# Kernel tuning notes

Hardware: AMD Instinct MI355X
Metric: run time of the kernel (lower is better)

## Reference

```python
import jax, jax.numpy as jnp
import numpy as np

S, R, CM, CZ, H = 128, 256, 256, 128, 8
HD = CM // H
INF = 1e9
EPS = 1e-5


def _ln(x, g, b):
    mu = jnp.mean(x, axis=-1, keepdims=True)
    var = jnp.var(x, axis=-1, keepdims=True)
    return (x - mu) * jax.lax.rsqrt(var + EPS) * g + b


def setup_inputs() -> dict:
    key = jax.random.key(0)
    ks = jax.random.split(key, 12)
    d = {
        'm': jax.random.normal(ks[0], (S, R, CM), jnp.float32),
        'z': jax.random.normal(ks[1], (R, R, CZ), jnp.float32),
        'mask': jnp.ones((S, R), jnp.float32),
        'ln_m_g': jnp.ones((CM,), jnp.float32),
        'ln_m_b': jnp.zeros((CM,), jnp.float32),
        'ln_z_g': jnp.ones((CZ,), jnp.float32),
        'ln_z_b': jnp.zeros((CZ,), jnp.float32),
        'w_z': jax.random.normal(ks[2], (CZ, H), jnp.float32) * 0.02,
        'wq': jax.random.normal(ks[3], (CM, CM), jnp.float32) * (1.0 / np.sqrt(CM)),
        'wk': jax.random.normal(ks[4], (CM, CM), jnp.float32) * (1.0 / np.sqrt(CM)),
        'wv': jax.random.normal(ks[5], (CM, CM), jnp.float32) * (1.0 / np.sqrt(CM)),
        'wg': jnp.zeros((CM, CM), jnp.float32),
        'bg': jnp.ones((CM,), jnp.float32),
        'wo': jax.random.normal(ks[6], (CM, CM), jnp.float32) * (1.0 / np.sqrt(CM)),
        'bo': jnp.zeros((CM,), jnp.float32),
    }
    return d


def reference(m, z, mask, ln_m_g, ln_m_b, ln_z_g, ln_z_b, w_z, wq, wk, wv, wg, bg, wo, bo):
    # pair bias: LN(z) -> per-head bias [H, R, R], broadcast over seq rows
    z_ln = _ln(z, ln_z_g, ln_z_b)
    pair_bias = jnp.einsum('ijc,ch->hij', z_ln, w_z)          # [H, R, R]
    mask_bias = (INF * (mask - 1.0))[:, None, None, :]        # [S, 1, 1, R]

    m_ln = _ln(m, ln_m_g, ln_m_b)                             # [S, R, CM]
    q = (m_ln @ wq).reshape(S, R, H, HD)
    k = (m_ln @ wk).reshape(S, R, H, HD)
    v = (m_ln @ wv).reshape(S, R, H, HD)

    scale = 1.0 / np.sqrt(HD).astype(np.float32)
    logits = jnp.einsum('sihd,sjhd->shij', q * scale, k)       # [S, H, R, R]
    logits = logits + pair_bias[None] + mask_bias
    attn = jax.nn.softmax(logits, axis=-1)

    o = jnp.einsum('shij,sjhd->sihd', attn, v).reshape(S, R, CM)
    g = jax.nn.sigmoid(m_ln @ wg + bg)
    return (g * o) @ wo + bo
```

## Files before the change

kernel.cpp:

```cpp
#include <hip/hip_runtime.h>
#include <hip/hip_bf16.h>

typedef unsigned short u16;
typedef __bf16 bf16x8 __attribute__((ext_vector_type(8)));
typedef float f32x4 __attribute__((ext_vector_type(4)));
typedef float f32x16 __attribute__((ext_vector_type(16)));
typedef unsigned short u16x8 __attribute__((ext_vector_type(8)));
typedef unsigned short u16x4 __attribute__((ext_vector_type(4)));

#define LOG2E 1.4426950408889634f

__device__ __forceinline__ u16 f2b(float f) {
  union { __bf16 b; u16 u; } v; v.b = (__bf16)f; return v.u;
}
__device__ __forceinline__ float bf2f(u16 u) {
  union { unsigned u; float f; } v; v.u = ((unsigned)u) << 16;
  return v.f;
}

__global__ __launch_bounds__(256) void k_pre(
    const float* __restrict__ wq, const float* __restrict__ wk,
    const float* __restrict__ wv, const float* __restrict__ wg,
    const float* __restrict__ wo, u16* __restrict__ wtp,
    const float* __restrict__ z, const float* __restrict__ zg,
    const float* __restrict__ zb, const float* __restrict__ wz,
    float* __restrict__ pbp,
    const float* __restrict__ m, const float* __restrict__ gam,
    const float* __restrict__ bet, u16* __restrict__ mln) {
  __shared__ float lt[64][68];
  const int b = blockIdx.x;
  const int t = threadIdx.x;
  if (b < 80) {
    const int widx = b >> 4;
    const int tid = b & 15;
    const int ri = (tid >> 2) * 64, ci = (tid & 3) * 64;
    const float* src = (widx == 0) ? wq : (widx == 1) ? wk : (widx == 2) ? wv
                      : (widx == 3) ? wg : wo;
    {
      const int r = t >> 2;
      #pragma unroll
      for (int i = 0; i < 4; ++i) {
        const int c = (t & 3) * 16 + i * 4;
        *(float4*)&lt[r][c] = *(const float4*)&src[(ri + r) * 256 + ci + c];
      }
    }
    __syncthreads();
    #pragma unroll
    for (int cc = 0; cc < 2; ++cc) {
      const int c = t + cc * 256;
      const int kb = c >> 8, cb = (c >> 6) & 3, lg = (c >> 4) & 3, lr = c & 15;
      u16x8 o;
      #pragma unroll
      for (int j = 0; j < 8; ++j) o[j] = f2b(lt[kb * 32 + lg * 8 + j][cb * 16 + lr]);
      const size_t idx = (size_t)widx * 65536 + (size_t)((ci >> 4) + cb) * 4096
                       + (size_t)((ri >> 5) + kb) * 512 + (size_t)(lg * 16 + lr) * 8;
      *(u16x8*)&wtp[idx] = o;
    }
  } else if (b < 4176) {
    const int lane = t & 63, wave = t >> 6;
    const int ql = lane & 15;
    const int p = (b - 80) * 16 + wave * 4 + (lane >> 4);
    const float4 zv0 = *(const float4*)(z + (size_t)p * 128 + ql * 8);
    const float4 zv1 = *(const float4*)(z + (size_t)p * 128 + ql * 8 + 4);
    float s = zv0.x + zv0.y + zv0.z + zv0.w + zv1.x + zv1.y + zv1.z + zv1.w;
    float sq = zv0.x * zv0.x + zv0.y * zv0.y + zv0.z * zv0.z + zv0.w * zv0.w
             + zv1.x * zv1.x + zv1.y * zv1.y + zv1.z * zv1.z + zv1.w * zv1.w;
    #pragma unroll
    for (int o = 8; o > 0; o >>= 1) { s += __shfl_xor(s, o); sq += __shfl_xor(sq, o); }
    const float mu = s * 0.0078125f;
    const float var = sq * 0.0078125f - mu * mu;
    const float rs = rsqrtf(var + 1e-5f);
    const int c0 = ql * 8;
    float zn[8];
    zn[0] = (zv0.x - mu) * rs * zg[c0 + 0] + zb[c0 + 0];
    zn[1] = (zv0.y - mu) * rs * zg[c0 + 1] + zb[c0 + 1];
    zn[2] = (zv0.z - mu) * rs * zg[c0 + 2] + zb[c0 + 2];
    zn[3] = (zv0.w - mu) * rs * zg[c0 + 3] + zb[c0 + 3];
    zn[4] = (zv1.x - mu) * rs * zg[c0 + 4] + zb[c0 + 4];
    zn[5] = (zv1.y - mu) * rs * zg[c0 + 5] + zb[c0 + 5];
    zn[6] = (zv1.z - mu) * rs * zg[c0 + 6] + zb[c0 + 6];
    zn[7] = (zv1.w - mu) * rs * zg[c0 + 7] + zb[c0 + 7];
    float a[8] = {};
    #pragma unroll
    for (int i = 0; i < 8; ++i) {
      #pragma unroll
      for (int hh = 0; hh < 8; ++hh) a[hh] += zn[i] * wz[(c0 + i) * 8 + hh];
    }
    #pragma unroll
    for (int hh = 0; hh < 8; ++hh) {
      #pragma unroll
      for (int o = 8; o > 0; o >>= 1) a[hh] += __shfl_xor(a[hh], o);
    }
    if (ql == 0) {
      const int i = p >> 8, j = p & 255;
      const int strip = i >> 5, il = i & 31, jt = j >> 5, r = j & 31;
      const int gh = (r >> 2) & 1, qd = r >> 3, c4 = r & 3;
      const int off = (strip * 8 + jt) * 1024 + (gh * 32 + il) * 16 + qd * 4 + c4;
      #pragma unroll
      for (int hh = 0; hh < 8; ++hh)
        pbp[(size_t)hh * 65536 + off] = a[hh] * LOG2E;
    }
  } else {
    const int lane = t & 63;
    const size_t row = (size_t)(b - 4176) * 4 + (t >> 6);
    const float4 xv = *(const float4*)(m + row * 256 + lane * 4);
    float s = xv.x + xv.y + xv.z + xv.w;
    float sq = xv.x * xv.x + xv.y * xv.y + xv.z * xv.z + xv.w * xv.w;
    #pragma unroll
    for (int o = 32; o > 0; o >>= 1) { s += __shfl_xor(s, o); sq += __shfl_xor(sq, o); }
    const float mu = s * 0.00390625f;
    const float var = sq * 0.00390625f - mu * mu;
    const float rs = rsqrtf(var + 1e-5f);
    const int c = lane * 4;
    u16x4 o4;
    o4.x = f2b((xv.x - mu) * rs * gam[c] + bet[c]);
    o4.y = f2b((xv.y - mu) * rs * gam[c + 1] + bet[c + 1]);
    o4.z = f2b((xv.z - mu) * rs * gam[c + 2] + bet[c + 2]);
    o4.w = f2b((xv.w - mu) * rs * gam[c + 3] + bet[c + 3]);
    *(u16x4*)(mln + row * 256 + c) = o4;
  }
}

__global__ __launch_bounds__(256, 2) void k_fused(
    const u16* __restrict__ mln, const u16* __restrict__ wtp,
    const float* __restrict__ bg, const float* __restrict__ pbp,
    const float* __restrict__ mask, u16* __restrict__ go) {
  __shared__ u16 lA[32 * 256];
  __shared__ u16 lQ[256 * 32];
  __shared__ u16 lK[256 * 32];
  __shared__ u16 lVt[32][276];
  __shared__ float lMb[256];
  __shared__ float lL[4][32];
  const int bid = blockIdx.x;
  const int s = bid & 127, h = bid >> 7;
  const int t = threadIdx.x;
  const int lane = t & 63, wave = t >> 6;
  const int il = lane & 31, gh = lane >> 5;

  const u16* Wb = wtp + (size_t)wave * 65536 + (size_t)(2 * h + (il >> 4)) * 4096
                + gh * 128 + (il & 15) * 8;
  bf16x8 B[16];
  #pragma unroll
  for (int kc = 0; kc < 16; ++kc) B[kc] = *(const bf16x8*)&Wb[kc * 256];
  __builtin_amdgcn_sched_barrier(0);

  lMb[t] = (LOG2E * 1e9f) * (mask[s * 256 + t] - 1.0f) - 24.0f;
  const float bgv = bg[h * 32 + il];
  const size_t mbase = (size_t)s * 65536;

  u16x8 areg[4];
  #pragma unroll
  for (int i = 0; i < 4; ++i)
    areg[i] = *(const u16x8*)&mln[mbase + (size_t)(i * 8 + (t >> 5)) * 256 + (t & 31) * 8];
  unsigned gpk[64];

  #pragma unroll
  for (int c = 0; c < 8; ++c) {
    #pragma unroll
    for (int i = 0; i < 4; ++i) {
      const int r = i * 8 + (t >> 5);
      *(u16x8*)((char*)lA + ((r * 512 + (t & 31) * 16) ^ ((r & 7) << 4))) = areg[i];
    }
    __syncthreads();
    if (c < 7) {
      #pragma unroll
      for (int i = 0; i < 4; ++i)
        areg[i] = *(const u16x8*)&mln[mbase +
            (size_t)((c + 1) * 32 + i * 8 + (t >> 5)) * 256 + (t & 31) * 8];
      __builtin_amdgcn_sched_barrier(0);
    }
    f32x16 a0 = {}, a1 = {};
    #pragma unroll
    for (int kc = 0; kc < 16; kc += 2) {
      const bf16x8 af0 = *(const bf16x8*)((const char*)lA +
          ((il * 512 + (kc * 16 + gh * 8) * 2) ^ ((il & 7) << 4)));
      const bf16x8 af1 = *(const bf16x8*)((const char*)lA +
          ((il * 512 + ((kc + 1) * 16 + gh * 8) * 2) ^ ((il & 7) << 4)));
      a0 = __builtin_amdgcn_mfma_f32_32x32x16_bf16(af0, B[kc], a0, 0, 0, 0);
      a1 = __builtin_amdgcn_mfma_f32_32x32x16_bf16(af1, B[kc + 1], a1, 0, 0, 0);
    }
    const f32x16 acc = a0 + a1;
    if (wave == 0) {
      #pragma unroll
      for (int reg = 0; reg < 16; ++reg) {
        const int R = c * 32 + (reg & 3) + 8 * (reg >> 2) + 4 * gh;
        *(u16*)((char*)lQ + ((R * 64 + il * 2) ^ ((R & 7) << 4))) =
            f2b(acc[reg] * (0.17677669529663687f * LOG2E));
      }
    } else if (wave == 1) {
      #pragma unroll
      for (int reg = 0; reg < 16; ++reg) {
        const int R = c * 32 + (reg & 3) + 8 * (reg >> 2) + 4 * gh;
        *(u16*)((char*)lK + ((R * 64 + il * 2) ^ ((R & 7) << 4))) = f2b(acc[reg]);
      }
    } else if (wave == 2) {
      #pragma unroll
      for (int reg = 0; reg < 16; ++reg) {
        const int R = c * 32 + (reg & 3) + 8 * (reg >> 2) + 4 * gh;
        lVt[il][R] = f2b(acc[reg]);
      }
    } else {
      #pragma unroll
      for (int r4 = 0; r4 < 8; ++r4) {
        const float x0 = acc[2 * r4] + bgv;
        const float x1 = acc[2 * r4 + 1] + bgv;
        const u16 u0 = f2b(1.0f / (1.0f + __expf(-x0)));
        const u16 u1 = f2b(1.0f / (1.0f + __expf(-x1)));
        gpk[c * 8 + r4] = (unsigned)u0 | ((unsigned)u1 << 16);
      }
    }
    __syncthreads();
  }

  if (wave == 3) {
    #pragma unroll
    for (int c = 0; c < 8; ++c) {
      #pragma unroll
      for (int r4 = 0; r4 < 8; ++r4) {
        const int R0 = c * 32 + ((2 * r4) & 3) + 8 * (r4 >> 1) + 4 * gh;
        const unsigned p = gpk[c * 8 + r4];
        lA[R0 * 32 + il] = (u16)p;
        lA[(R0 + 1) * 32 + il] = (u16)(p >> 16);
      }
    }
  }
  __syncthreads();

  #pragma unroll 1
  for (int strip = 0; strip < 2; ++strip) {
    const int i0 = wave * 64 + strip * 32;
    bf16x8 qf[2];
    #pragma unroll
    for (int kk = 0; kk < 2; ++kk) {
      const int row = i0 + il;
      qf[kk] = *(const bf16x8*)((const char*)lQ +
          ((row * 64 + (kk * 16 + gh * 8) * 2) ^ ((row & 7) << 4)));
    }
    const float* pbt = pbp + ((size_t)h * 8 + (i0 >> 5)) * 8192 + lane * 16;

    f32x16 oacc0 = {}, oacc1 = {};
    float s0 = 0.f, s1 = 0.f, s2 = 0.f, s3 = 0.f;

    #pragma unroll 2
    for (int jt = 0; jt < 8; ++jt) {
      const float* pl = pbt + jt * 1024;
      f32x16 c;
      #pragma unroll
      for (int qd = 0; qd < 4; ++qd) {
        const f32x4 pbq = *(const f32x4*)&pl[qd * 4];
        const int jb = jt * 32 + qd * 8 + gh * 4;
        #pragma unroll
        for (int c4 = 0; c4 < 4; ++c4)
          c[qd * 4 + c4] = pbq[c4] + lMb[jb + c4];
      }
      const int krow = jt * 32 + il;
      const bf16x8 kf0 = *(const bf16x8*)((const char*)lK +
          ((krow * 64 + (gh * 8) * 2) ^ ((krow & 7) << 4)));
      const bf16x8 kf1 = *(const bf16x8*)((const char*)lK +
          ((krow * 64 + (16 + gh * 8) * 2) ^ ((krow & 7) << 4)));
      c = __builtin_amdgcn_mfma_f32_32x32x16_bf16(kf0, qf[0], c, 0, 0, 0);
      c = __builtin_amdgcn_mfma_f32_32x32x16_bf16(kf1, qf[1], c, 0, 0, 0);
      union PK { __bf16 h[4]; uint2 u; } pk[4];
      #pragma unroll
      for (int qd = 0; qd < 4; ++qd) {
        const float p0 = exp2f(c[qd * 4 + 0]);
        const float p1 = exp2f(c[qd * 4 + 1]);
        const float p2 = exp2f(c[qd * 4 + 2]);
        const float p3 = exp2f(c[qd * 4 + 3]);
        s0 += p0; s1 += p1; s2 += p2; s3 += p3;
        pk[qd].h[0] = (__bf16)p0; pk[qd].h[1] = (__bf16)p1;
        pk[qd].h[2] = (__bf16)p2; pk[qd].h[3] = (__bf16)p3;
      }
      const uint2 sA = gh ? pk[0].u : pk[1].u;
      uint2 rA; rA.x = __shfl_xor(sA.x, 32); rA.y = __shfl_xor(sA.y, 32);
      const uint2 sB = gh ? pk[2].u : pk[3].u;
      uint2 rB; rB.x = __shfl_xor(sB.x, 32); rB.y = __shfl_xor(sB.y, 32);
      union FR { uint2 u2[2]; bf16x8 v; } fa0, fa1;
      fa0.u2[0] = gh ? rA : pk[0].u;
      fa0.u2[1] = gh ? pk[1].u : rA;
      fa1.u2[0] = gh ? rB : pk[2].u;
      fa1.u2[1] = gh ? pk[3].u : rB;
      const bf16x8 vf0 = *(const bf16x8*)&lVt[il][jt * 32 + gh * 8];
      const bf16x8 vf1 = *(const bf16x8*)&lVt[il][jt * 32 + 16 + gh * 8];
      oacc0 = __builtin_amdgcn_mfma_f32_32x32x16_bf16(fa0.v, vf0, oacc0, 0, 0, 0);
      oacc1 = __builtin_amdgcn_mfma_f32_32x32x16_bf16(fa1.v, vf1, oacc1, 0, 0, 0);
    }

    float lsum = (s0 + s1) + (s2 + s3);
    lsum += __shfl_xor(lsum, 32);
    if (lane < 32) lL[wave][il] = 1.0f / lsum;

    #pragma unroll
    for (int qd = 0; qd < 4; ++qd) {
      const f32x4 invq = *(const f32x4*)&lL[wave][qd * 8 + gh * 4];
      #pragma unroll
      for (int c4 = 0; c4 < 4; ++c4) {
        const int iloc = qd * 8 + gh * 4 + c4;
        const size_t row = (size_t)s * 256 + i0 + iloc;
        const int col = h * 32 + il;
        const float ov = (oacc0[qd * 4 + c4] + oacc1[qd * 4 + c4]) * invq[c4];
        const float gv = bf2f(lA[(i0 + iloc) * 32 + il]);
        go[row * 256 + col] = f2b(gv * ov);
      }
    }
  }
}

__global__ __launch_bounds__(256, 4) void k_gemm_out(
    const u16* __restrict__ go, const u16* __restrict__ wop,
    const float* __restrict__ bo, float* __restrict__ out) {
  __shared__ u16 lA[32 * 256];
  const int t = threadIdx.x;
  const size_t row0 = (size_t)blockIdx.x * 32;
  const int lane = t & 63, wave = t >> 6;
  const u16* Wz = wop + (size_t)wave * 16384 + (size_t)lane * 8;
  u16x8 areg[4];
  #pragma unroll
  for (int i = 0; i < 4; ++i)
    areg[i] = *(const u16x8*)&go[(row0 + i * 8 + (t >> 5)) * 256 + (t & 31) * 8];
  bf16x8 B[4][4];
  #pragma unroll
  for (int kc = 0; kc < 4; ++kc) {
    #pragma unroll
    for (int nn = 0; nn < 4; ++nn)
      B[kc][nn] = *(const bf16x8*)&Wz[nn * 4096 + kc * 512];
  }
  __builtin_amdgcn_sched_barrier(0);
  #pragma unroll
  for (int i = 0; i < 4; ++i) {
    const int r = i * 8 + (t >> 5);
    const int c = (t & 31) * 8;
    *(u16x8*)((char*)lA + ((r * 512 + c * 2) ^ ((r & 7) << 4))) = areg[i];
  }
  __syncthreads();
  const int lrow = lane & 15, lg = lane >> 4;
  f32x4 acc[2][4] = {};
  #pragma unroll
  for (int kc = 0; kc < 4; ++kc) {
    bf16x8 af[2];
    #pragma unroll
    for (int mm = 0; mm < 2; ++mm) {
      const int row = mm * 16 + lrow;
      af[mm] = *(const bf16x8*)((const char*)lA +
          ((row * 512 + kc * 64 + lg * 16) ^ ((row & 7) << 4)));
    }
    #pragma unroll
    for (int mm = 0; mm < 2; ++mm) {
      #pragma unroll
      for (int nn = 0; nn < 4; ++nn)
        acc[mm][nn] = __builtin_amdgcn_mfma_f32_16x16x32_bf16(
            af[mm], B[kc][nn], acc[mm][nn], 0, 0, 0);
    }
  }
  #pragma unroll
  for (int kc = 0; kc < 4; ++kc) {
    #pragma unroll
    for (int nn = 0; nn < 4; ++nn)
      B[kc][nn] = *(const bf16x8*)&Wz[nn * 4096 + (kc + 4) * 512];
  }
  __builtin_amdgcn_sched_barrier(0);
  #pragma unroll
  for (int kc = 0; kc < 4; ++kc) {
    bf16x8 af[2];
    #pragma unroll
    for (int mm = 0; mm < 2; ++mm) {
      const int row = mm * 16 + lrow;
      af[mm] = *(const bf16x8*)((const char*)lA +
          ((row * 512 + (kc + 4) * 64 + lg * 16) ^ ((row & 7) << 4)));
    }
    #pragma unroll
    for (int mm = 0; mm < 2; ++mm) {
      #pragma unroll
      for (int nn = 0; nn < 4; ++nn)
        acc[mm][nn] = __builtin_amdgcn_mfma_f32_16x16x32_bf16(
            af[mm], B[kc][nn], acc[mm][nn], 0, 0, 0);
    }
  }
  const int wc = wave * 64, lg4 = lg * 4;
  #pragma unroll
  for (int mm = 0; mm < 2; ++mm) {
    #pragma unroll
    for (int nn = 0; nn < 4; ++nn) {
      const int col = wc + nn * 16 + lrow;
      #pragma unroll
      for (int jr = 0; jr < 4; ++jr) {
        const size_t row = row0 + mm * 16 + lg4 + jr;
        out[row * 256 + col] = acc[mm][nn][jr] + bo[col];
      }
    }
  }
}

extern "C" void kernel_launch(void* const* d_in, const int* in_sizes, int n_in,
                              void* d_out, int out_size, void* d_ws, size_t ws_size,
                              hipStream_t stream) {
  const float* m      = (const float*)d_in[0];
  const float* z      = (const float*)d_in[1];
  const float* mask   = (const float*)d_in[2];
  const float* ln_m_g = (const float*)d_in[3];
  const float* ln_m_b = (const float*)d_in[4];
  const float* ln_z_g = (const float*)d_in[5];
  const float* ln_z_b = (const float*)d_in[6];
  const float* w_z    = (const float*)d_in[7];
  const float* wq     = (const float*)d_in[8];
  const float* wk     = (const float*)d_in[9];
  const float* wv     = (const float*)d_in[10];
  const float* wg     = (const float*)d_in[11];
  const float* bg     = (const float*)d_in[12];
  const float* wo     = (const float*)d_in[13];
  const float* bo     = (const float*)d_in[14];
  float* out = (float*)d_out;

  char* w = (char*)d_ws;
  u16* wtp   = (u16*)w;   w += (size_t)5 * 65536 * 2;
  float* pbp = (float*)w; w += (size_t)8 * 65536 * 4;
  u16* mln   = (u16*)w;   w += (size_t)32768 * 256 * 2;
  u16* gow   = (u16*)w;   w += (size_t)32768 * 256 * 2;

  k_pre      <<<12368, 256, 0, stream>>>(wq, wk, wv, wg, wo, wtp,
                                         z, ln_z_g, ln_z_b, w_z, pbp,
                                         m, ln_m_g, ln_m_b, mln);
  k_fused    <<<1024, 256, 0, stream>>>(mln, wtp, bg, pbp, mask, gow);
  k_gemm_out <<<1024, 256, 0, stream>>>(gow, wtp + (size_t)4 * 65536, bo, out);
}
```

Baseline: 114.4 us.

## Load projection A operands straight from global and spill gate to global memory

The fused attention kernel stops staging LayerNorm rows through a shared-memory tile and instead has each wave read its A fragments directly from global memory. The gate values are now written to a global scratch buffer rather than held in 64 registers and later in LDS. With LDS and register pressure lower, the launch bound rises from 2 to 3 blocks per SM. It also vectorizes the mask-bias LDS reads and uses the hardware exp2 builtin. The cost is that every wave reloads A redundantly from global or L2, and the gate makes an extra global round trip.

```diff
diff --git a/kernel.cpp b/kernel.cpp
--- a/kernel.cpp
+++ b/kernel.cpp
@@ -16,6 +16,9 @@
 __device__ __forceinline__ float bf2f(u16 u) {
   union { unsigned u; float f; } v; v.u = ((unsigned)u) << 16;
   return v.f;
+}
+__device__ __forceinline__ float fexp2(float x) {
+  return __builtin_amdgcn_exp2f(x);
 }
 
 __global__ __launch_bounds__(256) void k_pre(
@@ -121,11 +124,11 @@
   }
 }
 
-__global__ __launch_bounds__(256, 2) void k_fused(
+__global__ __launch_bounds__(256, 3) void k_fused(
     const u16* __restrict__ mln, const u16* __restrict__ wtp,
     const float* __restrict__ bg, const float* __restrict__ pbp,
-    const float* __restrict__ mask, u16* __restrict__ go) {
-  __shared__ u16 lA[32 * 256];
+    const float* __restrict__ mask, u16* __restrict__ g,
+    u16* __restrict__ go) {
   __shared__ u16 lQ[256 * 32];
   __shared__ u16 lK[256 * 32];
   __shared__ u16 lVt[32][276];
@@ -146,38 +149,19 @@
 
   lMb[t] = (LOG2E * 1e9f) * (mask[s * 256 + t] - 1.0f) - 24.0f;
   const float bgv = bg[h * 32 + il];
-  const size_t mbase = (size_t)s * 65536;
-
-  u16x8 areg[4];
-  #pragma unroll
-  for (int i = 0; i < 4; ++i)
-    areg[i] = *(const u16x8*)&mln[mbase + (size_t)(i * 8 + (t >> 5)) * 256 + (t & 31) * 8];
-  unsigned gpk[64];
+  const u16* Abase = mln + (size_t)s * 65536 + (size_t)il * 256 + gh * 8;
 
   #pragma unroll
   for (int c = 0; c < 8; ++c) {
-    #pragma unroll
-    for (int i = 0; i < 4; ++i) {
-      const int r = i * 8 + (t >> 5);
-      *(u16x8*)((char*)lA + ((r * 512 + (t & 31) * 16) ^ ((r & 7) << 4))) = areg[i];
-    }
-    __syncthreads();
-    if (c < 7) {
-      #pragma unroll
-      for (int i = 0; i < 4; ++i)
-        areg[i] = *(const u16x8*)&mln[mbase +
-            (size_t)((c + 1) * 32 + i * 8 + (t >> 5)) * 256 + (t & 31) * 8];
-      __builtin_amdgcn_sched_barrier(0);
-    }
+    bf16x8 A[16];
+    #pragma unroll
+    for (int kc = 0; kc < 16; ++kc)
+      A[kc] = *(const bf16x8*)&Abase[c * 8192 + kc * 16];
     f32x16 a0 = {}, a1 = {};
     #pragma unroll
     for (int kc = 0; kc < 16; kc += 2) {
-      const bf16x8 af0 = *(const bf16x8*)((const char*)lA +
-          ((il * 512 + (kc * 16 + gh * 8) * 2) ^ ((il & 7) << 4)));
-      const bf16x8 af1 = *(const bf16x8*)((const char*)lA +
-          ((il * 512 + ((kc + 1) * 16 + gh * 8) * 2) ^ ((il & 7) << 4)));
-      a0 = __builtin_amdgcn_mfma_f32_32x32x16_bf16(af0, B[kc], a0, 0, 0, 0);
-      a1 = __builtin_amdgcn_mfma_f32_32x32x16_bf16(af1, B[kc + 1], a1, 0, 0, 0);
+      a0 = __builtin_amdgcn_mfma_f32_32x32x16_bf16(A[kc], B[kc], a0, 0, 0, 0);
+      a1 = __builtin_amdgcn_mfma_f32_32x32x16_bf16(A[kc + 1], B[kc + 1], a1, 0, 0, 0);
     }
     const f32x16 acc = a0 + a1;
     if (wave == 0) {
@@ -201,26 +185,11 @@
       }
     } else {
       #pragma unroll
-      for (int r4 = 0; r4 < 8; ++r4) {
-        const float x0 = acc[2 * r4] + bgv;
-        const float x1 = acc[2 * r4 + 1] + bgv;
-        const u16 u0 = f2b(1.0f / (1.0f + __expf(-x0)));
-        const u16 u1 = f2b(1.0f / (1.0f + __expf(-x1)));
-        gpk[c * 8 + r4] = (unsigned)u0 | ((unsigned)u1 << 16);
-      }
-    }
-    __syncthreads();
-  }
-
-  if (wave == 3) {
-    #pragma unroll
-    for (int c = 0; c < 8; ++c) {
-      #pragma unroll
-      for (int r4 = 0; r4 < 8; ++r4) {
-        const int R0 = c * 32 + ((2 * r4) & 3) + 8 * (r4 >> 1) + 4 * gh;
-        const unsigned p = gpk[c * 8 + r4];
-        lA[R0 * 32 + il] = (u16)p;
-        lA[(R0 + 1) * 32 + il] = (u16)(p >> 16);
+      for (int reg = 0; reg < 16; ++reg) {
+        const int R = c * 32 + (reg & 3) + 8 * (reg >> 2) + 4 * gh;
+        const float x = acc[reg] + bgv;
+        g[(size_t)(s * 256 + R) * 256 + h * 32 + il] =
+            f2b(1.0f / (1.0f + __expf(-x)));
       }
     }
   }
@@ -248,10 +217,10 @@
       #pragma unroll
       for (int qd = 0; qd < 4; ++qd) {
         const f32x4 pbq = *(const f32x4*)&pl[qd * 4];
-        const int jb = jt * 32 + qd * 8 + gh * 4;
+        const f32x4 mb4 = *(const f32x4*)&lMb[jt * 32 + qd * 8 + gh * 4];
         #pragma unroll
         for (int c4 = 0; c4 < 4; ++c4)
-          c[qd * 4 + c4] = pbq[c4] + lMb[jb + c4];
+          c[qd * 4 + c4] = pbq[c4] + mb4[c4];
       }
       const int krow = jt * 32 + il;
       const bf16x8 kf0 = *(const bf16x8*)((const char*)lK +
@@ -263,10 +232,10 @@
       union PK { __bf16 h[4]; uint2 u; } pk[4];
       #pragma unroll
       for (int qd = 0; qd < 4; ++qd) {
-        const float p0 = exp2f(c[qd * 4 + 0]);
-        const float p1 = exp2f(c[qd * 4 + 1]);
-        const float p2 = exp2f(c[qd * 4 + 2]);
-        const float p3 = exp2f(c[qd * 4 + 3]);
+        const float p0 = fexp2(c[qd * 4 + 0]);
+        const float p1 = fexp2(c[qd * 4 + 1]);
+        const float p2 = fexp2(c[qd * 4 + 2]);
+        const float p3 = fexp2(c[qd * 4 + 3]);
         s0 += p0; s1 += p1; s2 += p2; s3 += p3;
         pk[qd].h[0] = (__bf16)p0; pk[qd].h[1] = (__bf16)p1;
         pk[qd].h[2] = (__bf16)p2; pk[qd].h[3] = (__bf16)p3;
@@ -299,7 +268,7 @@
         const size_t row = (size_t)s * 256 + i0 + iloc;
         const int col = h * 32 + il;
         const float ov = (oacc0[qd * 4 + c4] + oacc1[qd * 4 + c4]) * invq[c4];
-        const float gv = bf2f(lA[(i0 + iloc) * 32 + il]);
+        const float gv = bf2f(g[row * 256 + col]);
         go[row * 256 + col] = f2b(gv * ov);
       }
     }
@@ -416,10 +385,11 @@
   float* pbp = (float*)w; w += (size_t)8 * 65536 * 4;
   u16* mln   = (u16*)w;   w += (size_t)32768 * 256 * 2;
   u16* gow   = (u16*)w;   w += (size_t)32768 * 256 * 2;
+  u16* gw    = (u16*)w;   w += (size_t)32768 * 256 * 2;
 
   k_pre      <<<12368, 256, 0, stream>>>(wq, wk, wv, wg, wo, wtp,
                                          z, ln_z_g, ln_z_b, w_z, pbp,
                                          m, ln_m_g, ln_m_b, mln);
-  k_fused    <<<1024, 256, 0, stream>>>(mln, wtp, bg, pbp, mask, gow);
+  k_fused    <<<1024, 256, 0, stream>>>(mln, wtp, bg, pbp, mask, gw, gow);
   k_gemm_out <<<1024, 256, 0, stream>>>(gow, wtp + (size_t)4 * 65536, bo, out);
 }
```

Measured after the change: 149.4 us. +30.6%, slower.
